# Kernel optimization log

Hardware: AMD Instinct MI355X
Metric: run time of the kernel (lower is better)

Reference implementation:

```python
import jax, jax.numpy as jnp
import numpy as np

_DN = ('NCHW', 'OIHW', 'NCHW')

def _conv(x, w, stride=1, pad=1, dil=1, groups=1):
    return jax.lax.conv_general_dilated(
        x, w, window_strides=(stride, stride),
        padding=[(pad, pad), (pad, pad)],
        rhs_dilation=(dil, dil),
        feature_group_count=groups,
        dimension_numbers=_DN)


def setup_inputs() -> dict:
    key = jax.random.key(0)
    k1, k2, k3 = jax.random.split(key, 3)
    B, T, C_in, H, W = 4, 16, 32, 64, 64
    hidden = 64
    x = jax.random.normal(k1, (B, T, C_in, H, W), dtype=jnp.float32)
    # input-to-hidden conv weight: 3 gates stacked along out channels
    fan_i = C_in * 3 * 3
    W_i = jax.random.normal(k2, (3 * hidden, C_in, 3, 3), dtype=jnp.float32) / np.sqrt(fan_i)
    fan_h = hidden * 3 * 3
    W_h = jax.random.normal(k3, (3 * hidden, hidden, 3, 3), dtype=jnp.float32) / np.sqrt(fan_h)
    return {"x": x, "W_i": W_i, "W_h": W_h}


def reference(x, W_i, W_h):
    # x: [B, T, C_in, H, W] (batch_first). Single-layer unidirectional ConvGRU.
    B, T, C_in, H, Wd = x.shape
    hidden = W_h.shape[1]

    def cell(h, x_t):
        gi = _conv(x_t, W_i)          # [B, 3*hidden, H, W]
        gh = _conv(h, W_h)            # [B, 3*hidden, H, W]
        i_r, i_z, i_n = jnp.split(gi, 3, axis=1)
        h_r, h_z, h_n = jnp.split(gh, 3, axis=1)
        r = jax.nn.sigmoid(i_r + h_r)
        z = jax.nn.sigmoid(i_z + h_z)
        n = jnp.tanh(i_n + r * h_n)
        h_new = (1.0 - z) * n + z * h
        return h_new, h_new

    h0 = jnp.zeros((B, hidden, H, Wd), dtype=x.dtype)
    xs = jnp.moveaxis(x, 1, 0)        # [T, B, C_in, H, W]
    _, hs = jax.lax.scan(cell, h0, xs)
    return jnp.moveaxis(hs, 0, 1)     # [B, T, hidden, H, W]
```

## Files before the change

kernel.cpp:

```cpp
#include <hip/hip_runtime.h>
#include <math.h>

constexpr int B_  = 4;
constexpr int T_  = 16;
constexpr int CIN = 32;
constexpr int HID = 64;
constexpr int HH  = 64;
constexpr int WW  = 64;
constexpr int HW  = HH * WW;

constexpr int TR = 8,  TC = 16;
constexpr int PR = TR + 2, PC = TC + 2;
constexpr int CSL = 40;
constexpr int KCH = 32;
constexpr int ASLAB_HW  = 3 * 36 * 16 * 8;
constexpr int ATOTAL    = 12 * ASLAB_HW;
constexpr int TIN_HW    = PR * PC * CSL;
constexpr int TIN_GRAN  = TIN_HW / 8;
constexpr int ROW_HW    = 66 * CSL;
constexpr int PIMG_HW   = 66 * ROW_HW;

constexpr size_t A2_HW    = (size_t)ATOTAL;
constexpr size_t XT_OFF   = A2_HW;
constexpr size_t XT_HW    = (size_t)64 * PIMG_HW;
constexpr size_t HT_OFF   = XT_OFF + XT_HW;
constexpr size_t HTBUF_HW = (size_t)8 * PIMG_HW;
constexpr size_t WS_NEED_BYTES = (A2_HW + XT_HW + 2 * HTBUF_HW) * 2;

constexpr int PB_XFILL = 66 * 64;
constexpr int PB_WCONV = (ATOTAL + 255) / 256;
constexpr int HZ_GRAN  = (int)(2 * HTBUF_HW / 8);
constexpr int PB_HZERO = (HZ_GRAN + 255) / 256;
constexpr int PB_TOTAL = PB_XFILL + PB_WCONV + PB_HZERO;

typedef __attribute__((ext_vector_type(8))) short bf16x8;
typedef __attribute__((ext_vector_type(4))) float f32x4;

#define GLOAD_LDS16(gsrc, ldst) \
  __builtin_amdgcn_global_load_lds((const __attribute__((address_space(1))) void*)(gsrc), \
                                   (__attribute__((address_space(3))) void*)(ldst), 16, 0, 0)

__device__ inline unsigned short f2bf(float f) {
    union { float f; unsigned u; } v; v.f = f;
    return (unsigned short)((v.u + 0x7FFFu + ((v.u >> 16) & 1u)) >> 16);
}
__device__ inline float bf2f(unsigned short h) {
    union { unsigned u; float f; } v; v.u = (unsigned)h << 16; return v.f;
}

__global__ void prep(const float* __restrict__ x,
                     const float* __restrict__ Wi, const float* __restrict__ Wh,
                     unsigned short* __restrict__ A2,
                     unsigned short* __restrict__ xT,
                     unsigned short* __restrict__ hT) {
    __shared__ float lds[64 * 41];
    const int bid = blockIdx.x;

    if (bid < PB_XFILL) {
        const int riT = bid % 66;
        const int bt  = bid / 66;
        unsigned short* dst = xT + (size_t)bt * PIMG_HW + (size_t)riT * ROW_HW;
        const bool interior = (riT >= 1 && riT <= 64);
        if (interior) {
            const float* src = x + (size_t)bt * 32 * HW + (riT - 1) * WW;
            const int p = threadIdx.x & 63;
            #pragma unroll
            for (int j = 0; j < 8; ++j) {
                int c = j * 4 + (threadIdx.x >> 6);
                lds[p * 41 + c] = src[c * HW + p];
            }
        }
        __syncthreads();
        for (int g = threadIdx.x; g < ROW_HW / 8; g += 256) {
            bf16x8 vv;
            #pragma unroll
            for (int k = 0; k < 8; ++k) {
                int off = g * 8 + k;
                int px = off / CSL, slot = off - px * CSL;
                float v = 0.f;
                if (interior && slot < 32 && px >= 1 && px <= 64)
                    v = lds[(px - 1) * 41 + slot];
                vv[k] = (short)f2bf(v);
            }
            *(bf16x8*)(dst + g * 8) = vv;
        }
    } else if (bid < PB_XFILL + PB_WCONV) {
        int idx = (bid - PB_XFILL) * 256 + threadIdx.x;
        if (idx >= ATOTAL) return;
        int ic  = idx & 31;
        int r1  = idx >> 5;
        int tap = r1 % 9;
        int r2  = r1 / 9;
        int m   = r2 & 15;
        int r3  = r2 >> 4;
        int gt  = r3 % 3;
        int r4  = r3 / 3;
        int hg  = r4 & 3;
        int ch  = r4 >> 2;
        int o   = gt * 64 + hg * 16 + m;
        float w = (ch == 0) ? Wi[(o * CIN + ic) * 9 + tap]
                            : Wh[(o * HID + (ch - 1) * 32 + ic) * 9 + tap];
        size_t dst = (size_t)(ch * 4 + hg) * ASLAB_HW
                   + ((size_t)(gt * 36 + tap * 4 + (ic >> 3)) * 16 + m) * 8 + (ic & 7);
        A2[dst] = f2bf(w);
    } else {
        int i = (bid - PB_XFILL - PB_WCONV) * 256 + threadIdx.x;
        if (i < HZ_GRAN) ((f32x4*)hT)[i] = f32x4{0.f, 0.f, 0.f, 0.f};
    }
}

__global__ __launch_bounds__(256, 2) void convgru_mfma(
    const unsigned short* __restrict__ xT,
    const unsigned short* __restrict__ A2,
    const unsigned short* __restrict__ hTrd,
    unsigned short* __restrict__ hTwr,
    float* __restrict__ out, int t)
{
    __shared__ __align__(16) unsigned short t0s[TIN_HW];
    __shared__ __align__(16) unsigned short t1s[TIN_HW];
    __shared__ __align__(16) unsigned short t2s[TIN_HW];

    const int tid  = threadIdx.x;
    const int lane = tid & 63, wave = tid >> 6;
    const int px   = lane & 15, kl = lane >> 4;
    const int ty = blockIdx.x >> 2, tx = blockIdx.x & 3;
    const int hg = blockIdx.y, b = blockIdx.z;
    const int gy0 = ty * TR, gx0 = tx * TC;

    const unsigned short* xs = xT + (size_t)(b * T_ + t) * PIMG_HW;
    const int rowbase = gy0 * 66 + gx0;

    f32x4 accR[2] = {}, accZ[2] = {}, accNX[2] = {}, accNH[2] = {};
    bf16x8 a[27];

    auto stage_tin = [&](const unsigned short* src, unsigned short* dst) {
        #pragma unroll
        for (int j = 0; j < 4; ++j) {
            int G = tid + j * 256;
            if (G < TIN_GRAN) {
                int r = G / 90, w = G - 90 * r;
                GLOAD_LDS16(src + (size_t)(rowbase + r * 66) * CSL + w * 8, dst + G * 8);
            }
        }
    };
    auto regA = [&](int ch) {
        const unsigned short* s = A2 + (size_t)(ch * 4 + hg) * ASLAB_HW + lane * 8;
        #pragma unroll
        for (int i = 0; i < 27; ++i)
            a[i] = *(const bf16x8*)(s + (size_t)((i / 9) * 36 + (i % 9) * 4) * 128);
    };

    const int rb = (wave * 2 * PC + px) * CSL + kl * 8;

    auto compute = [&](const unsigned short* tb, bool isX, const unsigned short* nextA) {
        bf16x8 P[4][3];
        #pragma unroll
        for (int r = 0; r < 4; ++r)
            #pragma unroll
            for (int s = 0; s < 3; ++s)
                P[r][s] = *(const bf16x8*)(tb + rb + (r * PC + s) * CSL);
        #pragma unroll
        for (int dy = 0; dy < 3; ++dy) {
            #pragma unroll
            for (int dx = 0; dx < 3; ++dx) {
                const int tap = dy * 3 + dx;
                bf16x8 b0 = P[dy][dx], b1 = P[dy + 1][dx];
                bf16x8 ar = a[tap], az = a[9 + tap], an = a[18 + tap];
                if (nextA) {
                    a[tap]      = *(const bf16x8*)(nextA + (size_t)(0 * 36 + tap * 4) * 128);
                    a[9 + tap]  = *(const bf16x8*)(nextA + (size_t)(1 * 36 + tap * 4) * 128);
                    a[18 + tap] = *(const bf16x8*)(nextA + (size_t)(2 * 36 + tap * 4) * 128);
                }
                accR[0] = __builtin_amdgcn_mfma_f32_16x16x32_bf16(ar, b0, accR[0], 0, 0, 0);
                accR[1] = __builtin_amdgcn_mfma_f32_16x16x32_bf16(ar, b1, accR[1], 0, 0, 0);
                accZ[0] = __builtin_amdgcn_mfma_f32_16x16x32_bf16(az, b0, accZ[0], 0, 0, 0);
                accZ[1] = __builtin_amdgcn_mfma_f32_16x16x32_bf16(az, b1, accZ[1], 0, 0, 0);
                if (isX) {
                    accNX[0] = __builtin_amdgcn_mfma_f32_16x16x32_bf16(an, b0, accNX[0], 0, 0, 0);
                    accNX[1] = __builtin_amdgcn_mfma_f32_16x16x32_bf16(an, b1, accNX[1], 0, 0, 0);
                } else {
                    accNH[0] = __builtin_amdgcn_mfma_f32_16x16x32_bf16(an, b0, accNH[0], 0, 0, 0);
                    accNH[1] = __builtin_amdgcn_mfma_f32_16x16x32_bf16(an, b1, accNH[1], 0, 0, 0);
                }
            }
        }
    };

    stage_tin(xs, t0s);
    if (t > 0) {
        stage_tin(hTrd + (size_t)(b * 2 + 0) * PIMG_HW, t1s);
        stage_tin(hTrd + (size_t)(b * 2 + 1) * PIMG_HW, t2s);
    }
    regA(0);
    __syncthreads();

    const unsigned short* A1p = (t > 0)
        ? A2 + (size_t)(1 * 4 + hg) * ASLAB_HW + lane * 8 : nullptr;
    const unsigned short* A2p = (t > 0)
        ? A2 + (size_t)(2 * 4 + hg) * ASLAB_HW + lane * 8 : nullptr;

    compute(t0s, true, A1p);
    if (t > 0) {
        compute(t1s, false, A2p);
        compute(t2s, false, nullptr);
    }

    float* outp = out + ((size_t)(b * T_ + t)) * HID * HW;
    const int c0   = hg * 16 + kl * 4;
    const int slot = c0 & 31;
    const unsigned short* hbuf = (hg < 2) ? t1s : t2s;
    #pragma unroll
    for (int g = 0; g < 2; ++g) {
        int gy = gy0 + wave * 2 + g;
        int gx = gx0 + px;
        float hvf[4] = {0.f, 0.f, 0.f, 0.f};
        if (t > 0) {
            const unsigned short* hp =
                hbuf + ((wave * 2 + g + 1) * PC + (px + 1)) * CSL + slot;
            #pragma unroll
            for (int q = 0; q < 4; ++q) hvf[q] = bf2f(hp[q]);
        }
        unsigned short hvals[4];
        #pragma unroll
        for (int q = 0; q < 4; ++q) {
            int c = c0 + q;
            float sr = __builtin_amdgcn_rcpf(1.f + __expf(-accR[g][q]));
            float sz = __builtin_amdgcn_rcpf(1.f + __expf(-accZ[g][q]));
            float ag = accNX[g][q] + sr * accNH[g][q];
            float nn = 2.f * __builtin_amdgcn_rcpf(1.f + __expf(-2.f * ag)) - 1.f;
            float hn = nn + sz * (hvf[q] - nn);
            outp[(size_t)c * HW + gy * WW + gx] = hn;
            hvals[q] = f2bf(hn);
        }
        unsigned short* hd = hTwr + (size_t)(b * 2 + (c0 >> 5)) * PIMG_HW
                           + (size_t)((gy + 1) * 66 + (gx + 1)) * CSL + slot;
        *(uint2*)hd = *(const uint2*)hvals;
    }
}

constexpr int F_AROWB = 640;
constexpr int R4_ASLAB = 48 * 9 * KCH;
constexpr int R4_AVEC  = R4_ASLAB / 8;
constexpr int R4_ATOT  = 12 * R4_ASLAB;
__global__ void wconv_r4(const float* __restrict__ Wi, const float* __restrict__ Wh,
                         unsigned short* __restrict__ A2) {
    int idx = blockIdx.x * 256 + threadIdx.x;
    if (idx >= R4_ATOT) return;
    int ic = idx & 31; int r1 = idx >> 5;
    int tap = r1 % 9; int r2 = r1 / 9;
    int m = r2 & 15; int r3 = r2 >> 4;
    int gt = r3 % 3; int r4 = r3 / 3;
    int hg = r4 & 3; int ch = r4 >> 2;
    int o = gt * 64 + hg * 16 + m;
    float w = (ch == 0) ? Wi[(o * CIN + ic) * 9 + tap]
                        : Wh[(o * HID + (ch - 1) * 32 + ic) * 9 + tap];
    A2[idx] = f2bf(w);
}
__global__ __launch_bounds__(256, 2) void convgru_r4(
    const float* __restrict__ x, const unsigned short* __restrict__ A2,
    const float* hall, float* out, int t)
{
    __shared__ __align__(16) unsigned short tin[PR * PC * 40];
    __shared__ __align__(16) unsigned short Alr[48 * (F_AROWB / 2)];
    const int tid = threadIdx.x;
    const int lane = tid & 63, wave = tid >> 6;
    const int px = lane & 15, kl = lane >> 4;
    const int ty = blockIdx.x >> 2, tx = blockIdx.x & 3;
    const int hg = blockIdx.y, b = blockIdx.z;
    const int gy0 = ty * TR, gx0 = tx * TC;
    const int nch = (t > 0) ? 3 : 1;
    const float* hb = (t > 0) ? (hall + ((size_t)(b * T_ + t - 1)) * HID * HW) : nullptr;
    const float* xb = x + ((size_t)(b * T_ + t)) * CIN * HW;
    f32x4 accR[2] = {}, accZ[2] = {}, accNX[2] = {}, accNH[2] = {};
    float ireg[23]; bf16x8 areg[7];
    auto load_in = [&](int ch) {
        const float* src = (ch == 0) ? xb : (hb + (size_t)(ch - 1) * KCH * HW);
        #pragma unroll
        for (int j = 0; j < 23; ++j) {
            int e = tid + j * 256; float v = 0.f;
            if (e < PR * PC * KCH) {
                int ic = e / (PR * PC); int rem = e - ic * (PR * PC);
                int r = rem / PC, c = rem - r * PC;
                int gy = gy0 + r - 1, gx = gx0 + c - 1;
                if ((unsigned)gy < (unsigned)HH && (unsigned)gx < (unsigned)WW)
                    v = src[ic * HW + gy * WW + gx];
            }
            ireg[j] = v;
        }
    };
    auto load_Ar = [&](int ch) {
        const unsigned short* s = A2 + (size_t)(ch * 4 + hg) * R4_ASLAB;
        #pragma unroll
        for (int j = 0; j < 7; ++j) { int v = tid + j * 256; if (v < R4_AVEC) areg[j] = *(const bf16x8*)(s + v * 8); }
    };
    auto write_in = [&]() {
        #pragma unroll
        for (int j = 0; j < 23; ++j) {
            int e = tid + j * 256;
            if (e < PR * PC * KCH) {
                int ic = e / (PR * PC); int rem = e - ic * (PR * PC);
                int r = rem / PC, c = rem - r * PC;
                tin[(r * PC + c) * 40 + ic] = f2bf(ireg[j]);
            }
        }
    };
    auto write_Ar = [&]() {
        #pragma unroll
        for (int j = 0; j < 7; ++j) {
            int v = tid + j * 256;
            if (v < R4_AVEC) {
                int row = v / 36; int kb = (v - row * 36) * 16;
                char* dst = (char*)Alr + row * F_AROWB + (kb ^ ((row & 7) << 4));
                *(bf16x8*)dst = areg[j];
            }
        }
    };
    const int rb0 = ((wave * 2 + 0) * PC + px) * 40 + kl * 8;
    const int rb1 = rb0 + PC * 40;
    const int swA = (px & 7) << 4;
    auto compute = [&](bool isX) {
        #pragma unroll
        for (int tap = 0; tap < 9; ++tap) {
            const int dy = tap / 3, dx = tap - 3 * dy;
            const int toff = (dy * PC + dx) * 40;
            bf16x8 b0 = *(const bf16x8*)(tin + rb0 + toff);
            bf16x8 b1 = *(const bf16x8*)(tin + rb1 + toff);
            const char* ab = (const char*)Alr + px * F_AROWB + ((tap * 64 + kl * 16) ^ swA);
            bf16x8 ar = *(const bf16x8*)(ab);
            bf16x8 az = *(const bf16x8*)(ab + 16 * F_AROWB);
            bf16x8 an = *(const bf16x8*)(ab + 32 * F_AROWB);
            accR[0] = __builtin_amdgcn_mfma_f32_16x16x32_bf16(ar, b0, accR[0], 0, 0, 0);
            accR[1] = __builtin_amdgcn_mfma_f32_16x16x32_bf16(ar, b1, accR[1], 0, 0, 0);
            accZ[0] = __builtin_amdgcn_mfma_f32_16x16x32_bf16(az, b0, accZ[0], 0, 0, 0);
            accZ[1] = __builtin_amdgcn_mfma_f32_16x16x32_bf16(az, b1, accZ[1], 0, 0, 0);
            if (isX) {
                accNX[0] = __builtin_amdgcn_mfma_f32_16x16x32_bf16(an, b0, accNX[0], 0, 0, 0);
                accNX[1] = __builtin_amdgcn_mfma_f32_16x16x32_bf16(an, b1, accNX[1], 0, 0, 0);
            } else {
                accNH[0] = __builtin_amdgcn_mfma_f32_16x16x32_bf16(an, b0, accNH[0], 0, 0, 0);
                accNH[1] = __builtin_amdgcn_mfma_f32_16x16x32_bf16(an, b1, accNH[1], 0, 0, 0);
            }
        }
    };
    load_in(0); load_Ar(0); write_in(); write_Ar();
    __syncthreads();
    for (int ch = 0; ch < nch; ++ch) {
        if (ch + 1 < nch) { load_in(ch + 1); load_Ar(ch + 1); }
        compute(ch == 0);
        __syncthreads();
        if (ch + 1 < nch) { write_in(); write_Ar(); __syncthreads(); }
    }
    float* outp = out + ((size_t)(b * T_ + t)) * HID * HW;
    #pragma unroll
    for (int g = 0; g < 2; ++g) {
        int gy = gy0 + wave * 2 + g; int gx = gx0 + px;
        #pragma unroll
        for (int q = 0; q < 4; ++q) {
            int c = hg * 16 + kl * 4 + q;
            float sr = 1.f / (1.f + expf(-accR[g][q]));
            float sz = 1.f / (1.f + expf(-accZ[g][q]));
            float nn = tanhf(accNX[g][q] + sr * accNH[g][q]);
            float hv = hb ? hb[(size_t)c * HW + gy * WW + gx] : 0.f;
            outp[(size_t)c * HW + gy * WW + gx] = (1.f - sz) * nn + sz * hv;
        }
    }
}

extern "C" void kernel_launch(void* const* d_in, const int* in_sizes, int n_in,
                              void* d_out, int out_size, void* d_ws, size_t ws_size,
                              hipStream_t stream) {
    const float* x  = (const float*)d_in[0];
    const float* Wi = (const float*)d_in[1];
    const float* Wh = (const float*)d_in[2];
    float* out = (float*)d_out;

    if (ws_size >= WS_NEED_BYTES) {
        unsigned short* A2  = (unsigned short*)d_ws;
        unsigned short* xT  = A2 + XT_OFF;
        unsigned short* hT0 = A2 + HT_OFF;
        unsigned short* hT1 = hT0 + HTBUF_HW;

        prep<<<PB_TOTAL, 256, 0, stream>>>(x, Wi, Wh, A2, xT, hT0);
        for (int t = 0; t < T_; ++t) {
            unsigned short* rd = (t & 1) ? hT1 : hT0;
            unsigned short* wr = (t & 1) ? hT0 : hT1;
            convgru_mfma<<<dim3(32, 4, 4), 256, 0, stream>>>(xT, A2, rd, wr, out, t);
        }
    } else {
        unsigned short* A2 = (unsigned short*)d_ws;
        wconv_r4<<<(R4_ATOT + 255) / 256, 256, 0, stream>>>(Wi, Wh, A2);
        for (int t = 0; t < T_; ++t)
            convgru_r4<<<dim3(32, 4, 4), 256, 0, stream>>>(x, A2, out, out, t);
    }
}
```

Baseline: 166.7 us.

## Share input tile across all hidden groups per block with 4x16 spatial tiles

```diff
diff --git a/kernel.cpp b/kernel.cpp
--- a/kernel.cpp
+++ b/kernel.cpp
@@ -1,5 +1,9 @@
 #include <hip/hip_runtime.h>
 #include <math.h>
+
+typedef unsigned short us;
+typedef __attribute__((ext_vector_type(8))) short bf16x8;
+typedef __attribute__((ext_vector_type(4))) float f32x4;
 
 constexpr int B_  = 4;
 constexpr int T_  = 16;
@@ -9,23 +13,20 @@
 constexpr int WW  = 64;
 constexpr int HW  = HH * WW;
 
-constexpr int TR = 8,  TC = 16;
-constexpr int PR = TR + 2, PC = TC + 2;
 constexpr int CSL = 40;
 constexpr int KCH = 32;
-constexpr int ASLAB_HW  = 3 * 36 * 16 * 8;
-constexpr int ATOTAL    = 12 * ASLAB_HW;
-constexpr int TIN_HW    = PR * PC * CSL;
-constexpr int TIN_GRAN  = TIN_HW / 8;
-constexpr int ROW_HW    = 66 * CSL;
-constexpr int PIMG_HW   = 66 * ROW_HW;
-
-constexpr size_t A2_HW    = (size_t)ATOTAL;
-constexpr size_t XT_OFF   = A2_HW;
+constexpr int ASLAB_HW = 3 * 36 * 16 * 8;
+constexpr int ATOTAL   = 12 * ASLAB_HW;
+constexpr int ROW_HW   = 66 * CSL;
+constexpr int PIMG_HW  = 66 * ROW_HW;
+constexpr int T6_HW  = 6 * 18 * CSL;
+constexpr int T6_GR  = T6_HW / 8;
+
+constexpr size_t XT_OFF   = (size_t)ATOTAL;
 constexpr size_t XT_HW    = (size_t)64 * PIMG_HW;
 constexpr size_t HT_OFF   = XT_OFF + XT_HW;
 constexpr size_t HTBUF_HW = (size_t)8 * PIMG_HW;
-constexpr size_t WS_NEED_BYTES = (A2_HW + XT_HW + 2 * HTBUF_HW) * 2;
+constexpr size_t WS_NEED_BYTES = (HT_OFF + 2 * HTBUF_HW) * 2;
 
 constexpr int PB_XFILL = 66 * 64;
 constexpr int PB_WCONV = (ATOTAL + 255) / 256;
@@ -33,33 +34,29 @@
 constexpr int PB_HZERO = (HZ_GRAN + 255) / 256;
 constexpr int PB_TOTAL = PB_XFILL + PB_WCONV + PB_HZERO;
 
-typedef __attribute__((ext_vector_type(8))) short bf16x8;
-typedef __attribute__((ext_vector_type(4))) float f32x4;
-
 #define GLOAD_LDS16(gsrc, ldst) \
   __builtin_amdgcn_global_load_lds((const __attribute__((address_space(1))) void*)(gsrc), \
                                    (__attribute__((address_space(3))) void*)(ldst), 16, 0, 0)
-
-__device__ inline unsigned short f2bf(float f) {
+#define MFMA_B(d, A, Bv) d = __builtin_amdgcn_mfma_f32_16x16x32_bf16(A, Bv, d, 0, 0, 0)
+
+__device__ inline us f2bf(float f) {
     union { float f; unsigned u; } v; v.f = f;
-    return (unsigned short)((v.u + 0x7FFFu + ((v.u >> 16) & 1u)) >> 16);
-}
-__device__ inline float bf2f(unsigned short h) {
+    return (us)((v.u + 0x7FFFu + ((v.u >> 16) & 1u)) >> 16);
+}
+__device__ inline float bf2f(us h) {
     union { unsigned u; float f; } v; v.u = (unsigned)h << 16; return v.f;
 }
 
 __global__ void prep(const float* __restrict__ x,
                      const float* __restrict__ Wi, const float* __restrict__ Wh,
-                     unsigned short* __restrict__ A2,
-                     unsigned short* __restrict__ xT,
-                     unsigned short* __restrict__ hT) {
+                     us* __restrict__ A2, us* __restrict__ xT, us* __restrict__ hT) {
     __shared__ float lds[64 * 41];
     const int bid = blockIdx.x;
 
     if (bid < PB_XFILL) {
         const int riT = bid % 66;
         const int bt  = bid / 66;
-        unsigned short* dst = xT + (size_t)bt * PIMG_HW + (size_t)riT * ROW_HW;
+        us* dst = xT + (size_t)bt * PIMG_HW + (size_t)riT * ROW_HW;
         const bool interior = (riT >= 1 && riT <= 64);
         if (interior) {
             const float* src = x + (size_t)bt * 32 * HW + (riT - 1) * WW;
@@ -109,84 +106,80 @@
     }
 }
 
-__global__ __launch_bounds__(256, 2) void convgru_mfma(
-    const unsigned short* __restrict__ xT,
-    const unsigned short* __restrict__ A2,
-    const unsigned short* __restrict__ hTrd,
-    unsigned short* __restrict__ hTwr,
+__global__ __launch_bounds__(256, 1) void convgru_step(
+    const us* __restrict__ xT, const us* __restrict__ A2,
+    const us* __restrict__ hTrd, us* __restrict__ hTwr,
     float* __restrict__ out, int t)
 {
-    __shared__ __align__(16) unsigned short t0s[TIN_HW];
-    __shared__ __align__(16) unsigned short t1s[TIN_HW];
-    __shared__ __align__(16) unsigned short t2s[TIN_HW];
+    __shared__ __align__(16) us t0s[T6_HW];
+    __shared__ __align__(16) us t1s[T6_HW];
+    __shared__ __align__(16) us t2s[T6_HW];
 
     const int tid  = threadIdx.x;
-    const int lane = tid & 63, wave = tid >> 6;
+    const int lane = tid & 63, hg = tid >> 6;
     const int px   = lane & 15, kl = lane >> 4;
-    const int ty = blockIdx.x >> 2, tx = blockIdx.x & 3;
-    const int hg = blockIdx.y, b = blockIdx.z;
-    const int gy0 = ty * TR, gx0 = tx * TC;
-
-    const unsigned short* xs = xT + (size_t)(b * T_ + t) * PIMG_HW;
+    const int tile = blockIdx.x, ty = tile >> 2, tx = tile & 3, b = blockIdx.z;
+    const int gy0 = ty * 4, gx0 = tx * 16;
     const int rowbase = gy0 * 66 + gx0;
 
-    f32x4 accR[2] = {}, accZ[2] = {}, accNX[2] = {}, accNH[2] = {};
+    f32x4 aR[2][2], aZ[2][2], aNX[2][2], aNH[2][2];
+    #pragma unroll
+    for (int u = 0; u < 2; ++u)
+        #pragma unroll
+        for (int g = 0; g < 2; ++g) {
+            aR[u][g] = f32x4{0.f,0.f,0.f,0.f}; aZ[u][g] = f32x4{0.f,0.f,0.f,0.f};
+            aNX[u][g] = f32x4{0.f,0.f,0.f,0.f}; aNH[u][g] = f32x4{0.f,0.f,0.f,0.f};
+        }
     bf16x8 a[27];
 
-    auto stage_tin = [&](const unsigned short* src, unsigned short* dst) {
-        #pragma unroll
-        for (int j = 0; j < 4; ++j) {
+    auto stage_tin = [&](const us* src, us* dst) {
+        #pragma unroll
+        for (int j = 0; j < 3; ++j) {
             int G = tid + j * 256;
-            if (G < TIN_GRAN) {
+            if (G < T6_GR) {
                 int r = G / 90, w = G - 90 * r;
                 GLOAD_LDS16(src + (size_t)(rowbase + r * 66) * CSL + w * 8, dst + G * 8);
             }
         }
     };
     auto regA = [&](int ch) {
-        const unsigned short* s = A2 + (size_t)(ch * 4 + hg) * ASLAB_HW + lane * 8;
+        const us* s = A2 + (size_t)(ch * 4 + hg) * ASLAB_HW + lane * 8;
         #pragma unroll
         for (int i = 0; i < 27; ++i)
             a[i] = *(const bf16x8*)(s + (size_t)((i / 9) * 36 + (i % 9) * 4) * 128);
     };
 
-    const int rb = (wave * 2 * PC + px) * CSL + kl * 8;
-
-    auto compute = [&](const unsigned short* tb, bool isX, const unsigned short* nextA) {
-        bf16x8 P[4][3];
-        #pragma unroll
-        for (int r = 0; r < 4; ++r)
-            #pragma unroll
-            for (int s = 0; s < 3; ++s)
-                P[r][s] = *(const bf16x8*)(tb + rb + (r * PC + s) * CSL);
-        #pragma unroll
-        for (int dy = 0; dy < 3; ++dy) {
-            #pragma unroll
-            for (int dx = 0; dx < 3; ++dx) {
+    const int rbase = px * CSL + kl * 8;
+
+    auto compute = [&](const us* tb, bool isX, const us* nextA) {
+        #pragma unroll
+        for (int dx = 0; dx < 3; ++dx) {
+            bf16x8 P[6];
+            #pragma unroll
+            for (int r = 0; r < 6; ++r)
+                P[r] = *(const bf16x8*)(tb + (r * 18 + dx) * CSL + rbase);
+            #pragma unroll
+            for (int dy = 0; dy < 3; ++dy) {
                 const int tap = dy * 3 + dx;
-                bf16x8 b0 = P[dy][dx], b1 = P[dy + 1][dx];
                 bf16x8 ar = a[tap], az = a[9 + tap], an = a[18 + tap];
                 if (nextA) {
                     a[tap]      = *(const bf16x8*)(nextA + (size_t)(0 * 36 + tap * 4) * 128);
                     a[9 + tap]  = *(const bf16x8*)(nextA + (size_t)(1 * 36 + tap * 4) * 128);
                     a[18 + tap] = *(const bf16x8*)(nextA + (size_t)(2 * 36 + tap * 4) * 128);
                 }
-                accR[0] = __builtin_amdgcn_mfma_f32_16x16x32_bf16(ar, b0, accR[0], 0, 0, 0);
-                accR[1] = __builtin_amdgcn_mfma_f32_16x16x32_bf16(ar, b1, accR[1], 0, 0, 0);
-                accZ[0] = __builtin_amdgcn_mfma_f32_16x16x32_bf16(az, b0, accZ[0], 0, 0, 0);
-                accZ[1] = __builtin_amdgcn_mfma_f32_16x16x32_bf16(az, b1, accZ[1], 0, 0, 0);
-                if (isX) {
-                    accNX[0] = __builtin_amdgcn_mfma_f32_16x16x32_bf16(an, b0, accNX[0], 0, 0, 0);
-                    accNX[1] = __builtin_amdgcn_mfma_f32_16x16x32_bf16(an, b1, accNX[1], 0, 0, 0);
-                } else {
-                    accNH[0] = __builtin_amdgcn_mfma_f32_16x16x32_bf16(an, b0, accNH[0], 0, 0, 0);
-                    accNH[1] = __builtin_amdgcn_mfma_f32_16x16x32_bf16(an, b1, accNH[1], 0, 0, 0);
+                #pragma unroll
+                for (int u = 0; u < 2; ++u) {
+                    bf16x8 b0 = P[2 * u + dy], b1 = P[2 * u + dy + 1];
+                    MFMA_B(aR[u][0], ar, b0); MFMA_B(aR[u][1], ar, b1);
+                    MFMA_B(aZ[u][0], az, b0); MFMA_B(aZ[u][1], az, b1);
+                    if (isX) { MFMA_B(aNX[u][0], an, b0); MFMA_B(aNX[u][1], an, b1); }
+                    else     { MFMA_B(aNH[u][0], an, b0); MFMA_B(aNH[u][1], an, b1); }
                 }
             }
         }
     };
 
-    stage_tin(xs, t0s);
+    stage_tin(xT + (size_t)(b * T_ + t) * PIMG_HW, t0s);
     if (t > 0) {
         stage_tin(hTrd + (size_t)(b * 2 + 0) * PIMG_HW, t1s);
         stage_tin(hTrd + (size_t)(b * 2 + 1) * PIMG_HW, t2s);
@@ -194,10 +187,8 @@
     regA(0);
     __syncthreads();
 
-    const unsigned short* A1p = (t > 0)
-        ? A2 + (size_t)(1 * 4 + hg) * ASLAB_HW + lane * 8 : nullptr;
-    const unsigned short* A2p = (t > 0)
-        ? A2 + (size_t)(2 * 4 + hg) * ASLAB_HW + lane * 8 : nullptr;
+    const us* A1p = (t > 0) ? A2 + (size_t)(1 * 4 + hg) * ASLAB_HW + lane * 8 : nullptr;
+    const us* A2p = (t > 0) ? A2 + (size_t)(2 * 4 + hg) * ASLAB_HW + lane * 8 : nullptr;
 
     compute(t0s, true, A1p);
     if (t > 0) {
@@ -208,33 +199,34 @@
     float* outp = out + ((size_t)(b * T_ + t)) * HID * HW;
     const int c0   = hg * 16 + kl * 4;
     const int slot = c0 & 31;
-    const unsigned short* hbuf = (hg < 2) ? t1s : t2s;
+    const us* hbuf = (hg < 2) ? t1s : t2s;
     #pragma unroll
-    for (int g = 0; g < 2; ++g) {
-        int gy = gy0 + wave * 2 + g;
-        int gx = gx0 + px;
-        float hvf[4] = {0.f, 0.f, 0.f, 0.f};
-        if (t > 0) {
-            const unsigned short* hp =
-                hbuf + ((wave * 2 + g + 1) * PC + (px + 1)) * CSL + slot;
-            #pragma unroll
-            for (int q = 0; q < 4; ++q) hvf[q] = bf2f(hp[q]);
-        }
-        unsigned short hvals[4];
-        #pragma unroll
-        for (int q = 0; q < 4; ++q) {
-            int c = c0 + q;
-            float sr = __builtin_amdgcn_rcpf(1.f + __expf(-accR[g][q]));
-            float sz = __builtin_amdgcn_rcpf(1.f + __expf(-accZ[g][q]));
-            float ag = accNX[g][q] + sr * accNH[g][q];
-            float nn = 2.f * __builtin_amdgcn_rcpf(1.f + __expf(-2.f * ag)) - 1.f;
-            float hn = nn + sz * (hvf[q] - nn);
-            outp[(size_t)c * HW + gy * WW + gx] = hn;
-            hvals[q] = f2bf(hn);
-        }
-        unsigned short* hd = hTwr + (size_t)(b * 2 + (c0 >> 5)) * PIMG_HW
-                           + (size_t)((gy + 1) * 66 + (gx + 1)) * CSL + slot;
-        *(uint2*)hd = *(const uint2*)hvals;
+    for (int u = 0; u < 2; ++u) {
+        #pragma unroll
+        for (int g = 0; g < 2; ++g) {
+            int orow = 2 * u + g;
+            int gy = gy0 + orow, gx = gx0 + px;
+            float hvf[4] = {0.f, 0.f, 0.f, 0.f};
+            if (t > 0) {
+                const us* hp = hbuf + (size_t)((orow + 1) * 18 + (px + 1)) * CSL + slot;
+                #pragma unroll
+                for (int q = 0; q < 4; ++q) hvf[q] = bf2f(hp[q]);
+            }
+            us hv[4];
+            #pragma unroll
+            for (int q = 0; q < 4; ++q) {
+                float sr = __builtin_amdgcn_rcpf(1.f + __expf(-aR[u][g][q]));
+                float sz = __builtin_amdgcn_rcpf(1.f + __expf(-aZ[u][g][q]));
+                float ag = aNX[u][g][q] + sr * aNH[u][g][q];
+                float nn = 2.f * __builtin_amdgcn_rcpf(1.f + __expf(-2.f * ag)) - 1.f;
+                float hn = nn + sz * (hvf[q] - nn);
+                outp[(size_t)(c0 + q) * HW + gy * WW + gx] = hn;
+                hv[q] = f2bf(hn);
+            }
+            us* hd = hTwr + (size_t)(b * 2 + (c0 >> 5)) * PIMG_HW
+                   + (size_t)((gy + 1) * 66 + (gx + 1)) * CSL + slot;
+            *(uint2*)hd = *(const uint2*)hv;
+        }
     }
 }
 
@@ -242,8 +234,9 @@
 constexpr int R4_ASLAB = 48 * 9 * KCH;
 constexpr int R4_AVEC  = R4_ASLAB / 8;
 constexpr int R4_ATOT  = 12 * R4_ASLAB;
+constexpr int FPR = 10, FPC = 18;
 __global__ void wconv_r4(const float* __restrict__ Wi, const float* __restrict__ Wh,
-                         unsigned short* __restrict__ A2) {
+                         us* __restrict__ A2) {
     int idx = blockIdx.x * 256 + threadIdx.x;
     if (idx >= R4_ATOT) return;
     int ic = idx & 31; int r1 = idx >> 5;
@@ -257,30 +250,30 @@
     A2[idx] = f2bf(w);
 }
 __global__ __launch_bounds__(256, 2) void convgru_r4(
-    const float* __restrict__ x, const unsigned short* __restrict__ A2,
+    const float* __restrict__ x, const us* __restrict__ A2,
     const float* hall, float* out, int t)
 {
-    __shared__ __align__(16) unsigned short tin[PR * PC * 40];
-    __shared__ __align__(16) unsigned short Alr[48 * (F_AROWB / 2)];
+    __shared__ __align__(16) us tin[FPR * FPC * 40];
+    __shared__ __align__(16) us Alr[48 * (F_AROWB / 2)];
     const int tid = threadIdx.x;
     const int lane = tid & 63, wave = tid >> 6;
     const int px = lane & 15, kl = lane >> 4;
     const int ty = blockIdx.x >> 2, tx = blockIdx.x & 3;
     const int hg = blockIdx.y, b = blockIdx.z;
-    const int gy0 = ty * TR, gx0 = tx * TC;
+    const int gy0 = ty * 8, gx0 = tx * 16;
     const int nch = (t > 0) ? 3 : 1;
     const float* hb = (t > 0) ? (hall + ((size_t)(b * T_ + t - 1)) * HID * HW) : nullptr;
     const float* xb = x + ((size_t)(b * T_ + t)) * CIN * HW;
     f32x4 accR[2] = {}, accZ[2] = {}, accNX[2] = {}, accNH[2] = {};
     float ireg[23]; bf16x8 areg[7];
     auto load_in = [&](int ch) {
-        const float* src = (ch == 0) ? xb : (hb + (size_t)(ch - 1) * KCH * HW);
+        const float* src = (ch == 0) ? xb : (hb + (size_t)(ch - 1) * 32 * HW);
         #pragma unroll
         for (int j = 0; j < 23; ++j) {
             int e = tid + j * 256; float v = 0.f;
-            if (e < PR * PC * KCH) {
-                int ic = e / (PR * PC); int rem = e - ic * (PR * PC);
-                int r = rem / PC, c = rem - r * PC;
+            if (e < FPR * FPC * 32) {
+                int ic = e / (FPR * FPC); int rem = e - ic * (FPR * FPC);
+                int r = rem / FPC, c = rem - r * FPC;
                 int gy = gy0 + r - 1, gx = gx0 + c - 1;
                 if ((unsigned)gy < (unsigned)HH && (unsigned)gx < (unsigned)WW)
                     v = src[ic * HW + gy * WW + gx];
@@ -289,7 +282,7 @@
         }
     };
     auto load_Ar = [&](int ch) {
-        const unsigned short* s = A2 + (size_t)(ch * 4 + hg) * R4_ASLAB;
+        const us* s = A2 + (size_t)(ch * 4 + hg) * R4_ASLAB;
         #pragma unroll
         for (int j = 0; j < 7; ++j) { int v = tid + j * 256; if (v < R4_AVEC) areg[j] = *(const bf16x8*)(s + v * 8); }
     };
@@ -297,10 +290,10 @@
         #pragma unroll
         for (int j = 0; j < 23; ++j) {
             int e = tid + j * 256;
-            if (e < PR * PC * KCH) {
-                int ic = e / (PR * PC); int rem = e - ic * (PR * PC);
-                int r = rem / PC, c = rem - r * PC;
-                tin[(r * PC + c) * 40 + ic] = f2bf(ireg[j]);
+            if (e < FPR * FPC * 32) {
+                int ic = e / (FPR * FPC); int rem = e - ic * (FPR * FPC);
+                int r = rem / FPC, c = rem - r * FPC;
+                tin[(r * FPC + c) * 40 + ic] = f2bf(ireg[j]);
             }
         }
     };
@@ -315,31 +308,24 @@
             }
         }
     };
-    const int rb0 = ((wave * 2 + 0) * PC + px) * 40 + kl * 8;
-    const int rb1 = rb0 + PC * 40;
+    const int rb0 = ((wave * 2 + 0) * FPC + px) * 40 + kl * 8;
+    const int rb1 = rb0 + FPC * 40;
     const int swA = (px & 7) << 4;
     auto compute = [&](bool isX) {
         #pragma unroll
         for (int tap = 0; tap < 9; ++tap) {
             const int dy = tap / 3, dx = tap - 3 * dy;
-            const int toff = (dy * PC + dx) * 40;
+            const int toff = (dy * FPC + dx) * 40;
             bf16x8 b0 = *(const bf16x8*)(tin + rb0 + toff);
             bf16x8 b1 = *(const bf16x8*)(tin + rb1 + toff);
             const char* ab = (const char*)Alr + px * F_AROWB + ((tap * 64 + kl * 16) ^ swA);
             bf16x8 ar = *(const bf16x8*)(ab);
             bf16x8 az = *(const bf16x8*)(ab + 16 * F_AROWB);
             bf16x8 an = *(const bf16x8*)(ab + 32 * F_AROWB);
-            accR[0] = __builtin_amdgcn_mfma_f32_16x16x32_bf16(ar, b0, accR[0], 0, 0, 0);
-            accR[1] = __builtin_amdgcn_mfma_f32_16x16x32_bf16(ar, b1, accR[1], 0, 0, 0);
-            accZ[0] = __builtin_amdgcn_mfma_f32_16x16x32_bf16(az, b0, accZ[0], 0, 0, 0);
-            accZ[1] = __builtin_amdgcn_mfma_f32_16x16x32_bf16(az, b1, accZ[1], 0, 0, 0);
-            if (isX) {
-                accNX[0] = __builtin_amdgcn_mfma_f32_16x16x32_bf16(an, b0, accNX[0], 0, 0, 0);
-                accNX[1] = __builtin_amdgcn_mfma_f32_16x16x32_bf16(an, b1, accNX[1], 0, 0, 0);
-            } else {
-                accNH[0] = __builtin_amdgcn_mfma_f32_16x16x32_bf16(an, b0, accNH[0], 0, 0, 0);
-                accNH[1] = __builtin_amdgcn_mfma_f32_16x16x32_bf16(an, b1, accNH[1], 0, 0, 0);
-            }
+            MFMA_B(accR[0], ar, b0); MFMA_B(accR[1], ar, b1);
+            MFMA_B(accZ[0], az, b0); MFMA_B(accZ[1], az, b1);
+            if (isX) { MFMA_B(accNX[0], an, b0); MFMA_B(accNX[1], an, b1); }
+            else     { MFMA_B(accNH[0], an, b0); MFMA_B(accNH[1], an, b1); }
         }
     };
     load_in(0); load_Ar(0); write_in(); write_Ar();
@@ -375,19 +361,19 @@
     float* out = (float*)d_out;
 
     if (ws_size >= WS_NEED_BYTES) {
-        unsigned short* A2  = (unsigned short*)d_ws;
-        unsigned short* xT  = A2 + XT_OFF;
-        unsigned short* hT0 = A2 + HT_OFF;
-        unsigned short* hT1 = hT0 + HTBUF_HW;
+        us* A2  = (us*)d_ws;
+        us* xT  = A2 + XT_OFF;
+        us* hT0 = A2 + HT_OFF;
+        us* hT1 = hT0 + HTBUF_HW;
 
         prep<<<PB_TOTAL, 256, 0, stream>>>(x, Wi, Wh, A2, xT, hT0);
         for (int t = 0; t < T_; ++t) {
-            unsigned short* rd = (t & 1) ? hT1 : hT0;
-            unsigned short* wr = (t & 1) ? hT0 : hT1;
-            convgru_mfma<<<dim3(32, 4, 4), 256, 0, stream>>>(xT, A2, rd, wr, out, t);
+            us* rd = (t & 1) ? hT1 : hT0;
+            us* wr = (t & 1) ? hT0 : hT1;
+            convgru_step<<<dim3(64, 1, 4), 256, 0, stream>>>(xT, A2, rd, wr, out, t);
         }
     } else {
-        unsigned short* A2 = (unsigned short*)d_ws;
+        us* A2 = (us*)d_ws;
         wconv_r4<<<(R4_ATOT + 255) / 256, 256, 0, stream>>>(Wi, Wh, A2);
         for (int t = 0; t < T_; ++t)
             convgru_r4<<<dim3(32, 4, 4), 256, 0, stream>>>(x, A2, out, out, t);
```

After: 152.3 us. -8.6%, faster.
